# Optimization experiments

Hardware: AMD Instinct MI355X
Metric: run time of the kernel (lower is better)

Reference implementation:

```python
import jax, jax.numpy as jnp
import numpy as np

WORLD_SIZE = 8
BS = 16
MSG = 16384


def setup_inputs() -> dict:
    key = jax.random.key(0)
    k0, k1, kw, kb = jax.random.split(key, 4)
    x0 = jax.random.normal(k0, (WORLD_SIZE, BS, MSG), dtype=jnp.float32)
    x1 = jax.random.normal(k1, (WORLD_SIZE, BS, MSG), dtype=jnp.float32)
    # nn.Linear(msg_size, msg_size) params, kaiming-uniform-ish scale
    scale = 1.0 / np.sqrt(MSG)
    W = jax.random.uniform(kw, (MSG, MSG), dtype=jnp.float32, minval=-scale, maxval=scale)
    b = jax.random.uniform(kb, (MSG,), dtype=jnp.float32, minval=-scale, maxval=scale)
    return {"x0": x0, "x1": x1, "W": W, "b": b}


def reference(x0, x1, W, b):
    # all_gather_ll: concat per-rank shards along dim 0 -> [world_size*bs, msg]
    t0 = x0.reshape(WORLD_SIZE * BS, MSG)
    t1 = x1.reshape(WORLD_SIZE * BS, MSG)
    # shared Linear applied to both gathered tensors: y = t @ W^T + b
    y0 = jnp.einsum("nk,mk->nm", t0, W) + b
    y1 = jnp.einsum("nk,mk->nm", t1, W) + b
    return (y0, y1)
```

## Files before the change

### kernel.cpp

```cpp
#include <hip/hip_runtime.h>
#include <hip/hip_bf16.h>

typedef __bf16 bf16x8 __attribute__((ext_vector_type(8)));
typedef float  f32x4  __attribute__((ext_vector_type(4)));

#define N_TOT   16384
#define K_TOT   16384
#define HALF_M  ((size_t)128 * 16384)
#define BN      128
#define BK      64
#define KSPLIT  4
#define KQ_LEN  (K_TOT / KSPLIT)
#define NQSTEPS (KQ_LEN / BK)
#define OUT_ELEMS ((size_t)256 * 16384)

__device__ __forceinline__ unsigned short f2bf(float f) {
    __hip_bfloat16 h = __float2bfloat16(f);
    return __builtin_bit_cast(unsigned short, h);
}

__device__ __forceinline__ int swz(int row, int g) {
    return row * 128 + (((g ^ (row & 7)) & 7) << 4);
}

__global__ void cvtT_kernel(const float* __restrict__ x0,
                            const float* __restrict__ x1,
                            unsigned short* __restrict__ wsT) {
    size_t i = (size_t)blockIdx.x * blockDim.x + threadIdx.x;
    size_t e = i * 8;
    const float* src = (e < HALF_M) ? (x0 + e) : (x1 + (e - HALF_M));
    float4 a = ((const float4*)src)[0];
    float4 b = ((const float4*)src)[1];
    union { unsigned short u[8]; uint4 v; } o;
    o.u[0] = f2bf(a.x); o.u[1] = f2bf(a.y); o.u[2] = f2bf(a.z); o.u[3] = f2bf(a.w);
    o.u[4] = f2bf(b.x); o.u[5] = f2bf(b.y); o.u[6] = f2bf(b.z); o.u[7] = f2bf(b.w);
    ((uint4*)wsT)[i] = o.v;
}

__global__ void combine_kernel(float* __restrict__ out,
                               const float* __restrict__ p0,
                               const float* __restrict__ p1,
                               const float* __restrict__ p2) {
    const size_t n4 = OUT_ELEMS / 4;
    size_t i = (size_t)blockIdx.x * blockDim.x + threadIdx.x;
    for (; i < n4; i += (size_t)gridDim.x * blockDim.x) {
        float4 o = ((const float4*)out)[i];
        float4 a = ((const float4*)p0)[i];
        float4 b = ((const float4*)p1)[i];
        float4 c = ((const float4*)p2)[i];
        o.x += a.x + b.x + c.x;  o.y += a.y + b.y + c.y;
        o.z += a.z + b.z + c.z;  o.w += a.w + b.w + c.w;
        ((float4*)out)[i] = o;
    }
}

#define ISSUEW(S, k0) do {                                                    \
    const uint4* _p = (const uint4*)(arow_w + (k0));                          \
    w##S##_0 = _p[0]; w##S##_1 = _p[1];                                       \
    const f32x4* _q = (const f32x4*)(brow + (k0));                            \
    wb##S##_0 = __builtin_nontemporal_load(_q);                               \
    wb##S##_1 = __builtin_nontemporal_load(_q + 1);                           \
} while (0)

#define STAGEW(S, Ab, Bb) do {                                                \
    *(uint4*)((Ab) + aw0) = w##S##_0;                                         \
    *(uint4*)((Ab) + aw1) = w##S##_1;                                         \
    union { unsigned short u[8]; uint4 v; } _tb;                              \
    _tb.u[0]=f2bf(wb##S##_0[0]); _tb.u[1]=f2bf(wb##S##_0[1]);                 \
    _tb.u[2]=f2bf(wb##S##_0[2]); _tb.u[3]=f2bf(wb##S##_0[3]);                 \
    _tb.u[4]=f2bf(wb##S##_1[0]); _tb.u[5]=f2bf(wb##S##_1[1]);                 \
    _tb.u[6]=f2bf(wb##S##_1[2]); _tb.u[7]=f2bf(wb##S##_1[3]);                 \
    *(uint4*)((Bb) + bw) = _tb.v;                                             \
} while (0)

#define COMPUTE(Ab, Bb) do {                                                  \
    bf16x8 _b00 = *(const bf16x8*)((Bb) + boff00);                            \
    bf16x8 _b01 = *(const bf16x8*)((Bb) + boff01);                            \
    bf16x8 _b10 = *(const bf16x8*)((Bb) + boff10);                            \
    bf16x8 _b11 = *(const bf16x8*)((Bb) + boff11);                            \
    bf16x8 _a;                                                                \
    _a = *(const bf16x8*)((Ab) + aoff00);                                     \
    acc00 = __builtin_amdgcn_mfma_f32_16x16x32_bf16(_a, _b00, acc00, 0, 0, 0);\
    acc01 = __builtin_amdgcn_mfma_f32_16x16x32_bf16(_a, _b10, acc01, 0, 0, 0);\
    _a = *(const bf16x8*)((Ab) + aoff01);                                     \
    acc00 = __builtin_amdgcn_mfma_f32_16x16x32_bf16(_a, _b01, acc00, 0, 0, 0);\
    acc01 = __builtin_amdgcn_mfma_f32_16x16x32_bf16(_a, _b11, acc01, 0, 0, 0);\
    _a = *(const bf16x8*)((Ab) + aoff10);                                     \
    acc10 = __builtin_amdgcn_mfma_f32_16x16x32_bf16(_a, _b00, acc10, 0, 0, 0);\
    acc11 = __builtin_amdgcn_mfma_f32_16x16x32_bf16(_a, _b10, acc11, 0, 0, 0);\
    _a = *(const bf16x8*)((Ab) + aoff11);                                     \
    acc10 = __builtin_amdgcn_mfma_f32_16x16x32_bf16(_a, _b01, acc10, 0, 0, 0);\
    acc11 = __builtin_amdgcn_mfma_f32_16x16x32_bf16(_a, _b11, acc11, 0, 0, 0);\
    _a = *(const bf16x8*)((Ab) + aoff20);                                     \
    acc20 = __builtin_amdgcn_mfma_f32_16x16x32_bf16(_a, _b00, acc20, 0, 0, 0);\
    acc21 = __builtin_amdgcn_mfma_f32_16x16x32_bf16(_a, _b10, acc21, 0, 0, 0);\
    _a = *(const bf16x8*)((Ab) + aoff21);                                     \
    acc20 = __builtin_amdgcn_mfma_f32_16x16x32_bf16(_a, _b01, acc20, 0, 0, 0);\
    acc21 = __builtin_amdgcn_mfma_f32_16x16x32_bf16(_a, _b11, acc21, 0, 0, 0);\
    _a = *(const bf16x8*)((Ab) + aoff30);                                     \
    acc30 = __builtin_amdgcn_mfma_f32_16x16x32_bf16(_a, _b00, acc30, 0, 0, 0);\
    acc31 = __builtin_amdgcn_mfma_f32_16x16x32_bf16(_a, _b10, acc31, 0, 0, 0);\
    _a = *(const bf16x8*)((Ab) + aoff31);                                     \
    acc30 = __builtin_amdgcn_mfma_f32_16x16x32_bf16(_a, _b01, acc30, 0, 0, 0);\
    acc31 = __builtin_amdgcn_mfma_f32_16x16x32_bf16(_a, _b11, acc31, 0, 0, 0);\
} while (0)

#define SYNC do {                                                             \
    asm volatile("s_waitcnt lgkmcnt(0)" ::: "memory");                        \
    __builtin_amdgcn_s_barrier();                                             \
    __builtin_amdgcn_sched_barrier(0);                                        \
} while (0)

__global__ __launch_bounds__(1024, 4)
void gemm_ws(const float* __restrict__ W, const float* __restrict__ bias,
             const unsigned short* __restrict__ wsT,
             float* __restrict__ out, float* __restrict__ wsP)
{
    __shared__ uint4 smem_[(2 * 32768 + 2 * 16384) / 16];
    char* const sm = (char*)smem_;
    char* const A0 = sm;
    char* const A1 = sm + 32768;
    char* const B0 = sm + 65536;
    char* const B1 = sm + 65536 + 16384;

    const int tid  = threadIdx.x;
    const int lane = tid & 63;
    const int wave = tid >> 6;
    const int wm = wave >> 2;
    const int wn = wave & 3;
    const int bid    = blockIdx.x;
    const int kq     = bid >> 7;
    const int nstrip = bid & 127;
    const int n0     = nstrip * BN;
    const int kbase  = kq * KQ_LEN;

    const int ra  = tid >> 2;
    const int pa  = tid & 3;
    const int rbs = tid >> 3;

    const unsigned short* arow_w = wsT + (size_t)ra * K_TOT + kbase + pa * 16;
    const float* brow = W + (size_t)(n0 + rbs) * K_TOT + kbase + (tid & 7) * 8;

    const int aw0 = swz(ra, 2 * pa);
    const int aw1 = swz(ra, 2 * pa + 1);
    const int bw  = swz(rbs, tid & 7);

    const int aoff00 = swz(wm * 64 +  0 + (lane & 15), 0 + (lane >> 4));
    const int aoff01 = swz(wm * 64 +  0 + (lane & 15), 4 + (lane >> 4));
    const int aoff10 = swz(wm * 64 + 16 + (lane & 15), 0 + (lane >> 4));
    const int aoff11 = swz(wm * 64 + 16 + (lane & 15), 4 + (lane >> 4));
    const int aoff20 = swz(wm * 64 + 32 + (lane & 15), 0 + (lane >> 4));
    const int aoff21 = swz(wm * 64 + 32 + (lane & 15), 4 + (lane >> 4));
    const int aoff30 = swz(wm * 64 + 48 + (lane & 15), 0 + (lane >> 4));
    const int aoff31 = swz(wm * 64 + 48 + (lane & 15), 4 + (lane >> 4));
    const int boff00 = swz(wn * 32 +  0 + (lane & 15), 0 + (lane >> 4));
    const int boff01 = swz(wn * 32 +  0 + (lane & 15), 4 + (lane >> 4));
    const int boff10 = swz(wn * 32 + 16 + (lane & 15), 0 + (lane >> 4));
    const int boff11 = swz(wn * 32 + 16 + (lane & 15), 4 + (lane >> 4));

    f32x4 acc00 = {0.f,0.f,0.f,0.f}, acc01 = {0.f,0.f,0.f,0.f};
    f32x4 acc10 = {0.f,0.f,0.f,0.f}, acc11 = {0.f,0.f,0.f,0.f};
    f32x4 acc20 = {0.f,0.f,0.f,0.f}, acc21 = {0.f,0.f,0.f,0.f};
    f32x4 acc30 = {0.f,0.f,0.f,0.f}, acc31 = {0.f,0.f,0.f,0.f};

    uint4 w0_0, w0_1, w1_0, w1_1;
    f32x4 wb0_0, wb0_1, wb1_0, wb1_1;

    ISSUEW(0, 0);
    ISSUEW(1, BK);
    STAGEW(0, A0, B0);
    SYNC;

    for (int kt = 0; kt < NQSTEPS; kt += 2) {
        if (kt + 2 < NQSTEPS) ISSUEW(0, (kt + 2) * BK);
        COMPUTE(A0, B0);
        STAGEW(1, A1, B1);
        SYNC;
        if (kt + 3 < NQSTEPS) ISSUEW(1, (kt + 3) * BK);
        COMPUTE(A1, B1);
        if (kt + 2 < NQSTEPS) STAGEW(0, A0, B0);
        SYNC;
    }

    float* const dst = (kq == 0) ? out : (wsP + (size_t)(kq - 1) * OUT_ELEMS);
    #pragma unroll
    for (int nf = 0; nf < 2; ++nf) {
        const int col = n0 + wn * 32 + nf * 16 + (lane & 15);
        const float bv = (kq == 0) ? bias[col] : 0.f;
        #pragma unroll
        for (int mf = 0; mf < 4; ++mf) {
            const f32x4 a =
                (nf == 0) ? (mf == 0 ? acc00 : mf == 1 ? acc10 : mf == 2 ? acc20 : acc30)
                          : (mf == 0 ? acc01 : mf == 1 ? acc11 : mf == 2 ? acc21 : acc31);
            #pragma unroll
            for (int j = 0; j < 4; ++j) {
                int r = wm * 64 + mf * 16 + (lane >> 4) * 4 + j;
                float v = a[j] + bv;
                float* o = (r < 128) ? (dst + (size_t)r * N_TOT + col)
                                     : (dst + HALF_M + (size_t)(r - 128) * N_TOT + col);
                *o = v;
            }
        }
    }
}

extern "C" void kernel_launch(void* const* d_in, const int* in_sizes, int n_in,
                              void* d_out, int out_size, void* d_ws, size_t ws_size,
                              hipStream_t stream) {
    const float* x0 = (const float*)d_in[0];
    const float* x1 = (const float*)d_in[1];
    const float* W  = (const float*)d_in[2];
    const float* b  = (const float*)d_in[3];
    float* out = (float*)d_out;

    const size_t wsT_bytes = (size_t)256 * 16384 * sizeof(unsigned short);

    unsigned short* wsT = (unsigned short*)d_ws;
    float* wsP = (float*)((char*)d_ws + wsT_bytes);

    cvtT_kernel<<<2048, 256, 0, stream>>>(x0, x1, wsT);
    gemm_ws<<<512, 1024, 0, stream>>>(W, b, wsT, out, wsP);
    combine_kernel<<<2048, 256, 0, stream>>>(out, wsP, wsP + OUT_ELEMS,
                                             wsP + 2 * OUT_ELEMS);
}
```

Measured before the change: 310.6 us.

## Widen GEMM N-tile to 256 with 4x4 MFMA fragments per wave

Doubles the block N-tile to 256 columns, giving each wave a 64x64 output tile with 16 accumulators and halving the grid to 256 blocks, one per CU. Shared memory grows to 128KB, and the register prefetch pipeline drops to a single staged set loaded after the LDS write. The aim is better operand reuse per LDS read and fewer redundant activation loads, at the cost of higher register pressure and reduced prefetch depth for the fp32 weight stream.

```diff
diff --git a/kernel.cpp b/kernel.cpp
--- a/kernel.cpp
+++ b/kernel.cpp
@@ -7,7 +7,7 @@
 #define N_TOT   16384
 #define K_TOT   16384
 #define HALF_M  ((size_t)128 * 16384)
-#define BN      128
+#define BN      256
 #define BK      64
 #define KSPLIT  4
 #define KQ_LEN  (K_TOT / KSPLIT)
@@ -54,55 +54,60 @@
     }
 }
 
-#define ISSUEW(S, k0) do {                                                    \
+#define ISSUE(k0) do {                                                        \
     const uint4* _p = (const uint4*)(arow_w + (k0));                          \
-    w##S##_0 = _p[0]; w##S##_1 = _p[1];                                       \
+    aR0 = _p[0]; aR1 = _p[1];                                                 \
     const f32x4* _q = (const f32x4*)(brow + (k0));                            \
-    wb##S##_0 = __builtin_nontemporal_load(_q);                               \
-    wb##S##_1 = __builtin_nontemporal_load(_q + 1);                           \
-} while (0)
-
-#define STAGEW(S, Ab, Bb) do {                                                \
-    *(uint4*)((Ab) + aw0) = w##S##_0;                                         \
-    *(uint4*)((Ab) + aw1) = w##S##_1;                                         \
-    union { unsigned short u[8]; uint4 v; } _tb;                              \
-    _tb.u[0]=f2bf(wb##S##_0[0]); _tb.u[1]=f2bf(wb##S##_0[1]);                 \
-    _tb.u[2]=f2bf(wb##S##_0[2]); _tb.u[3]=f2bf(wb##S##_0[3]);                 \
-    _tb.u[4]=f2bf(wb##S##_1[0]); _tb.u[5]=f2bf(wb##S##_1[1]);                 \
-    _tb.u[6]=f2bf(wb##S##_1[2]); _tb.u[7]=f2bf(wb##S##_1[3]);                 \
-    *(uint4*)((Bb) + bw) = _tb.v;                                             \
+    wR0 = _q[0]; wR1 = _q[1]; wR2 = _q[2]; wR3 = _q[3];                       \
+} while (0)
+
+#define STAGE(Ab, Bb) do {                                                    \
+    *(uint4*)((Ab) + aw0) = aR0;                                              \
+    *(uint4*)((Ab) + aw1) = aR1;                                              \
+    union { unsigned short u[8]; uint4 v; } _t0, _t1;                         \
+    _t0.u[0]=f2bf(wR0[0]); _t0.u[1]=f2bf(wR0[1]);                             \
+    _t0.u[2]=f2bf(wR0[2]); _t0.u[3]=f2bf(wR0[3]);                             \
+    _t0.u[4]=f2bf(wR1[0]); _t0.u[5]=f2bf(wR1[1]);                             \
+    _t0.u[6]=f2bf(wR1[2]); _t0.u[7]=f2bf(wR1[3]);                             \
+    _t1.u[0]=f2bf(wR2[0]); _t1.u[1]=f2bf(wR2[1]);                             \
+    _t1.u[2]=f2bf(wR2[2]); _t1.u[3]=f2bf(wR2[3]);                             \
+    _t1.u[4]=f2bf(wR3[0]); _t1.u[5]=f2bf(wR3[1]);                             \
+    _t1.u[6]=f2bf(wR3[2]); _t1.u[7]=f2bf(wR3[3]);                             \
+    *(uint4*)((Bb) + bw0) = _t0.v;                                            \
+    *(uint4*)((Bb) + bw1) = _t1.v;                                            \
+} while (0)
+
+#define COMPUTE_HALF(Ab, Bb, AOFF, BOFF) do {                                 \
+    bf16x8 _a0 = *(const bf16x8*)((Ab) + (AOFF) + 0*2048);                    \
+    bf16x8 _a1 = *(const bf16x8*)((Ab) + (AOFF) + 1*2048);                    \
+    bf16x8 _a2 = *(const bf16x8*)((Ab) + (AOFF) + 2*2048);                    \
+    bf16x8 _a3 = *(const bf16x8*)((Ab) + (AOFF) + 3*2048);                    \
+    bf16x8 _bv;                                                               \
+    _bv = *(const bf16x8*)((Bb) + (BOFF) + 0*2048);                           \
+    acc00 = __builtin_amdgcn_mfma_f32_16x16x32_bf16(_a0, _bv, acc00, 0,0,0);  \
+    acc10 = __builtin_amdgcn_mfma_f32_16x16x32_bf16(_a1, _bv, acc10, 0,0,0);  \
+    acc20 = __builtin_amdgcn_mfma_f32_16x16x32_bf16(_a2, _bv, acc20, 0,0,0);  \
+    acc30 = __builtin_amdgcn_mfma_f32_16x16x32_bf16(_a3, _bv, acc30, 0,0,0);  \
+    _bv = *(const bf16x8*)((Bb) + (BOFF) + 1*2048);                           \
+    acc01 = __builtin_amdgcn_mfma_f32_16x16x32_bf16(_a0, _bv, acc01, 0,0,0);  \
+    acc11 = __builtin_amdgcn_mfma_f32_16x16x32_bf16(_a1, _bv, acc11, 0,0,0);  \
+    acc21 = __builtin_amdgcn_mfma_f32_16x16x32_bf16(_a2, _bv, acc21, 0,0,0);  \
+    acc31 = __builtin_amdgcn_mfma_f32_16x16x32_bf16(_a3, _bv, acc31, 0,0,0);  \
+    _bv = *(const bf16x8*)((Bb) + (BOFF) + 2*2048);                           \
+    acc02 = __builtin_amdgcn_mfma_f32_16x16x32_bf16(_a0, _bv, acc02, 0,0,0);  \
+    acc12 = __builtin_amdgcn_mfma_f32_16x16x32_bf16(_a1, _bv, acc12, 0,0,0);  \
+    acc22 = __builtin_amdgcn_mfma_f32_16x16x32_bf16(_a2, _bv, acc22, 0,0,0);  \
+    acc32 = __builtin_amdgcn_mfma_f32_16x16x32_bf16(_a3, _bv, acc32, 0,0,0);  \
+    _bv = *(const bf16x8*)((Bb) + (BOFF) + 3*2048);                           \
+    acc03 = __builtin_amdgcn_mfma_f32_16x16x32_bf16(_a0, _bv, acc03, 0,0,0);  \
+    acc13 = __builtin_amdgcn_mfma_f32_16x16x32_bf16(_a1, _bv, acc13, 0,0,0);  \
+    acc23 = __builtin_amdgcn_mfma_f32_16x16x32_bf16(_a2, _bv, acc23, 0,0,0);  \
+    acc33 = __builtin_amdgcn_mfma_f32_16x16x32_bf16(_a3, _bv, acc33, 0,0,0);  \
 } while (0)
 
 #define COMPUTE(Ab, Bb) do {                                                  \
-    bf16x8 _b00 = *(const bf16x8*)((Bb) + boff00);                            \
-    bf16x8 _b01 = *(const bf16x8*)((Bb) + boff01);                            \
-    bf16x8 _b10 = *(const bf16x8*)((Bb) + boff10);                            \
-    bf16x8 _b11 = *(const bf16x8*)((Bb) + boff11);                            \
-    bf16x8 _a;                                                                \
-    _a = *(const bf16x8*)((Ab) + aoff00);                                     \
-    acc00 = __builtin_amdgcn_mfma_f32_16x16x32_bf16(_a, _b00, acc00, 0, 0, 0);\
-    acc01 = __builtin_amdgcn_mfma_f32_16x16x32_bf16(_a, _b10, acc01, 0, 0, 0);\
-    _a = *(const bf16x8*)((Ab) + aoff01);                                     \
-    acc00 = __builtin_amdgcn_mfma_f32_16x16x32_bf16(_a, _b01, acc00, 0, 0, 0);\
-    acc01 = __builtin_amdgcn_mfma_f32_16x16x32_bf16(_a, _b11, acc01, 0, 0, 0);\
-    _a = *(const bf16x8*)((Ab) + aoff10);                                     \
-    acc10 = __builtin_amdgcn_mfma_f32_16x16x32_bf16(_a, _b00, acc10, 0, 0, 0);\
-    acc11 = __builtin_amdgcn_mfma_f32_16x16x32_bf16(_a, _b10, acc11, 0, 0, 0);\
-    _a = *(const bf16x8*)((Ab) + aoff11);                                     \
-    acc10 = __builtin_amdgcn_mfma_f32_16x16x32_bf16(_a, _b01, acc10, 0, 0, 0);\
-    acc11 = __builtin_amdgcn_mfma_f32_16x16x32_bf16(_a, _b11, acc11, 0, 0, 0);\
-    _a = *(const bf16x8*)((Ab) + aoff20);                                     \
-    acc20 = __builtin_amdgcn_mfma_f32_16x16x32_bf16(_a, _b00, acc20, 0, 0, 0);\
-    acc21 = __builtin_amdgcn_mfma_f32_16x16x32_bf16(_a, _b10, acc21, 0, 0, 0);\
-    _a = *(const bf16x8*)((Ab) + aoff21);                                     \
-    acc20 = __builtin_amdgcn_mfma_f32_16x16x32_bf16(_a, _b01, acc20, 0, 0, 0);\
-    acc21 = __builtin_amdgcn_mfma_f32_16x16x32_bf16(_a, _b11, acc21, 0, 0, 0);\
-    _a = *(const bf16x8*)((Ab) + aoff30);                                     \
-    acc30 = __builtin_amdgcn_mfma_f32_16x16x32_bf16(_a, _b00, acc30, 0, 0, 0);\
-    acc31 = __builtin_amdgcn_mfma_f32_16x16x32_bf16(_a, _b10, acc31, 0, 0, 0);\
-    _a = *(const bf16x8*)((Ab) + aoff31);                                     \
-    acc30 = __builtin_amdgcn_mfma_f32_16x16x32_bf16(_a, _b01, acc30, 0, 0, 0);\
-    acc31 = __builtin_amdgcn_mfma_f32_16x16x32_bf16(_a, _b11, acc31, 0, 0, 0);\
+    COMPUTE_HALF(Ab, Bb, aK0, bK0);                                           \
+    COMPUTE_HALF(Ab, Bb, aK1, bK1);                                           \
 } while (0)
 
 #define SYNC do {                                                             \
@@ -116,12 +121,12 @@
              const unsigned short* __restrict__ wsT,
              float* __restrict__ out, float* __restrict__ wsP)
 {
-    __shared__ uint4 smem_[(2 * 32768 + 2 * 16384) / 16];
+    __shared__ uint4 smem_[(4 * 32768) / 16];
     char* const sm = (char*)smem_;
     char* const A0 = sm;
     char* const A1 = sm + 32768;
     char* const B0 = sm + 65536;
-    char* const B1 = sm + 65536 + 16384;
+    char* const B1 = sm + 65536 + 32768;
 
     const int tid  = threadIdx.x;
     const int lane = tid & 63;
@@ -129,69 +134,63 @@
     const int wm = wave >> 2;
     const int wn = wave & 3;
     const int bid    = blockIdx.x;
-    const int kq     = bid >> 7;
-    const int nstrip = bid & 127;
+    const int kq     = bid >> 6;
+    const int nstrip = bid & 63;
     const int n0     = nstrip * BN;
     const int kbase  = kq * KQ_LEN;
 
-    const int ra  = tid >> 2;
-    const int pa  = tid & 3;
-    const int rbs = tid >> 3;
-
-    const unsigned short* arow_w = wsT + (size_t)ra * K_TOT + kbase + pa * 16;
-    const float* brow = W + (size_t)(n0 + rbs) * K_TOT + kbase + (tid & 7) * 8;
-
-    const int aw0 = swz(ra, 2 * pa);
-    const int aw1 = swz(ra, 2 * pa + 1);
-    const int bw  = swz(rbs, tid & 7);
-
-    const int aoff00 = swz(wm * 64 +  0 + (lane & 15), 0 + (lane >> 4));
-    const int aoff01 = swz(wm * 64 +  0 + (lane & 15), 4 + (lane >> 4));
-    const int aoff10 = swz(wm * 64 + 16 + (lane & 15), 0 + (lane >> 4));
-    const int aoff11 = swz(wm * 64 + 16 + (lane & 15), 4 + (lane >> 4));
-    const int aoff20 = swz(wm * 64 + 32 + (lane & 15), 0 + (lane >> 4));
-    const int aoff21 = swz(wm * 64 + 32 + (lane & 15), 4 + (lane >> 4));
-    const int aoff30 = swz(wm * 64 + 48 + (lane & 15), 0 + (lane >> 4));
-    const int aoff31 = swz(wm * 64 + 48 + (lane & 15), 4 + (lane >> 4));
-    const int boff00 = swz(wn * 32 +  0 + (lane & 15), 0 + (lane >> 4));
-    const int boff01 = swz(wn * 32 +  0 + (lane & 15), 4 + (lane >> 4));
-    const int boff10 = swz(wn * 32 + 16 + (lane & 15), 0 + (lane >> 4));
-    const int boff11 = swz(wn * 32 + 16 + (lane & 15), 4 + (lane >> 4));
-
-    f32x4 acc00 = {0.f,0.f,0.f,0.f}, acc01 = {0.f,0.f,0.f,0.f};
-    f32x4 acc10 = {0.f,0.f,0.f,0.f}, acc11 = {0.f,0.f,0.f,0.f};
-    f32x4 acc20 = {0.f,0.f,0.f,0.f}, acc21 = {0.f,0.f,0.f,0.f};
-    f32x4 acc30 = {0.f,0.f,0.f,0.f}, acc31 = {0.f,0.f,0.f,0.f};
-
-    uint4 w0_0, w0_1, w1_0, w1_1;
-    f32x4 wb0_0, wb0_1, wb1_0, wb1_1;
-
-    ISSUEW(0, 0);
-    ISSUEW(1, BK);
-    STAGEW(0, A0, B0);
+    const int rr = tid >> 2;
+    const int pp = tid & 3;
+
+    const unsigned short* arow_w = wsT + (size_t)rr * K_TOT + kbase + pp * 16;
+    const float* brow = W + (size_t)(n0 + rr) * K_TOT + kbase + pp * 16;
+
+    const int aw0 = swz(rr, 2 * pp);
+    const int aw1 = swz(rr, 2 * pp + 1);
+    const int bw0 = aw0;
+    const int bw1 = aw1;
+
+    const int aK0 = swz(wm * 64 + (lane & 15), lane >> 4);
+    const int aK1 = aK0 ^ 64;
+    const int bK0 = swz(wn * 64 + (lane & 15), lane >> 4);
+    const int bK1 = bK0 ^ 64;
+
+    f32x4 acc00={0,0,0,0}, acc01={0,0,0,0}, acc02={0,0,0,0}, acc03={0,0,0,0};
+    f32x4 acc10={0,0,0,0}, acc11={0,0,0,0}, acc12={0,0,0,0}, acc13={0,0,0,0};
+    f32x4 acc20={0,0,0,0}, acc21={0,0,0,0}, acc22={0,0,0,0}, acc23={0,0,0,0};
+    f32x4 acc30={0,0,0,0}, acc31={0,0,0,0}, acc32={0,0,0,0}, acc33={0,0,0,0};
+
+    uint4 aR0, aR1;
+    f32x4 wR0, wR1, wR2, wR3;
+
+    ISSUE(0);
+    STAGE(A0, B0);
+    ISSUE(BK);
     SYNC;
 
     for (int kt = 0; kt < NQSTEPS; kt += 2) {
-        if (kt + 2 < NQSTEPS) ISSUEW(0, (kt + 2) * BK);
         COMPUTE(A0, B0);
-        STAGEW(1, A1, B1);
+        STAGE(A1, B1);
+        if (kt + 2 < NQSTEPS) ISSUE((kt + 2) * BK);
         SYNC;
-        if (kt + 3 < NQSTEPS) ISSUEW(1, (kt + 3) * BK);
         COMPUTE(A1, B1);
-        if (kt + 2 < NQSTEPS) STAGEW(0, A0, B0);
+        if (kt + 2 < NQSTEPS) STAGE(A0, B0);
+        if (kt + 3 < NQSTEPS) ISSUE((kt + 3) * BK);
         SYNC;
     }
 
     float* const dst = (kq == 0) ? out : (wsP + (size_t)(kq - 1) * OUT_ELEMS);
     #pragma unroll
-    for (int nf = 0; nf < 2; ++nf) {
-        const int col = n0 + wn * 32 + nf * 16 + (lane & 15);
+    for (int nf = 0; nf < 4; ++nf) {
+        const int col = n0 + wn * 64 + nf * 16 + (lane & 15);
         const float bv = (kq == 0) ? bias[col] : 0.f;
         #pragma unroll
         for (int mf = 0; mf < 4; ++mf) {
             const f32x4 a =
-                (nf == 0) ? (mf == 0 ? acc00 : mf == 1 ? acc10 : mf == 2 ? acc20 : acc30)
-                          : (mf == 0 ? acc01 : mf == 1 ? acc11 : mf == 2 ? acc21 : acc31);
+                (nf == 0) ? (mf==0?acc00:mf==1?acc10:mf==2?acc20:acc30) :
+                (nf == 1) ? (mf==0?acc01:mf==1?acc11:mf==2?acc21:acc31) :
+                (nf == 2) ? (mf==0?acc02:mf==1?acc12:mf==2?acc22:acc32) :
+                            (mf==0?acc03:mf==1?acc13:mf==2?acc23:acc33);
             #pragma unroll
             for (int j = 0; j < 4; ++j) {
                 int r = wm * 64 + mf * 16 + (lane >> 4) * 4 + j;
@@ -219,7 +218,7 @@
     float* wsP = (float*)((char*)d_ws + wsT_bytes);
 
     cvtT_kernel<<<2048, 256, 0, stream>>>(x0, x1, wsT);
-    gemm_ws<<<512, 1024, 0, stream>>>(W, b, wsT, out, wsP);
+    gemm_ws<<<256, 1024, 0, stream>>>(W, b, wsT, out, wsP);
     combine_kernel<<<2048, 256, 0, stream>>>(out, wsP, wsP + OUT_ELEMS,
                                              wsP + 2 * OUT_ELEMS);
 }
```

Measured after the change: 467.5 us. 50.5% more time.
